# Kernel tuning notes

Measured on AMD Instinct MI355X. Metric: run time of the kernel, lower is better.

## Reference

```python
import jax, jax.numpy as jnp
import numpy as np

NUM_FEATURES = 35
BLANK = 2          # local blank index inside each 3-way category
NEG = -1e30        # finite stand-in for -inf (keeps grads NaN-free)


def _ctc_losses(log_probs, ext, skip_ok, valid, input_lengths, target_lengths):
    """Batched CTC negative log-likelihood.
    log_probs: [T,B,F,3] log-softmax per category
    ext:       [B,F,L] extended label sequence (blank interleaved), L=2S+1
    skip_ok:   [B,F,L] whether the l-2 transition is allowed
    valid:     [B,F,L] positions within 2*target_len+1
    Returns per-(B,F) loss.
    """
    T = log_probs.shape[0]

    emit0 = jnp.take_along_axis(log_probs[0], ext, axis=-1)  # [B,F,L]
    alpha = jnp.full_like(emit0, NEG)
    alpha = alpha.at[..., 0].set(emit0[..., 0])
    alpha = alpha.at[..., 1].set(jnp.where(target_lengths > 0, emit0[..., 1], NEG))

    pad1 = jnp.full(alpha.shape[:-1] + (1,), NEG, alpha.dtype)
    pad2 = jnp.full(alpha.shape[:-1] + (2,), NEG, alpha.dtype)

    def step(alpha, xs):
        lp_t, t = xs                                   # lp_t: [B,F,3]
        emit = jnp.take_along_axis(lp_t, ext, axis=-1)  # [B,F,L]
        a1 = jnp.concatenate([pad1, alpha[..., :-1]], axis=-1)
        a2 = jnp.concatenate([pad2, alpha[..., :-2]], axis=-1)
        prev = jnp.logaddexp(jnp.logaddexp(alpha, a1),
                             jnp.where(skip_ok, a2, NEG))
        new = jnp.where(valid, prev + emit, NEG)
        active = (t < input_lengths)[:, None, None]     # [B,1,1]
        return jnp.where(active, new, alpha), None

    alpha, _ = jax.lax.scan(step, alpha, (log_probs[1:], jnp.arange(1, T)))

    idx_last = 2 * target_lengths                       # [B,F] final blank
    last = jnp.take_along_axis(alpha, idx_last[..., None], axis=-1)[..., 0]
    prev_ = jnp.take_along_axis(alpha, jnp.maximum(idx_last - 1, 0)[..., None], axis=-1)[..., 0]
    prev_ = jnp.where(target_lengths > 0, prev_, NEG)
    ll = jnp.logaddexp(last, prev_)
    # zero_infinity=True: impossible alignments contribute 0 loss
    return jnp.where(ll > -1e29, -ll, 0.0)


def reference(logits, targets, input_lengths, target_lengths):
    # logits: [T,B,71]; targets: [B,35,S] local labels in {0,1};
    # input_lengths: [B]; target_lengths: [B,35]
    T, B, _ = logits.shape
    F = NUM_FEATURES
    pos = logits[:, :, :F]
    neg = logits[:, :, F:2 * F]
    blank = jnp.broadcast_to(logits[:, :, 2 * F:2 * F + 1], pos.shape)
    lp = jax.nn.log_softmax(jnp.stack([pos, neg, blank], axis=-1), axis=-1)  # [T,B,F,3]

    S = targets.shape[-1]
    L = 2 * S + 1
    ext = jnp.full((B, F, L), BLANK, jnp.int32).at[:, :, 1::2].set(targets.astype(jnp.int32))
    posL = jnp.arange(L)
    valid = posL[None, None, :] < (2 * target_lengths[..., None] + 1)
    ext_m2 = jnp.pad(ext[:, :, :-2], ((0, 0), (0, 0), (2, 0)), constant_values=BLANK)
    skip_ok = (ext != BLANK) & (ext != ext_m2) & (posL[None, None, :] >= 2)

    loss_bf = _ctc_losses(lp, ext, skip_ok, valid, input_lengths, target_lengths)  # [B,F]
    # reduction='mean': per-sample loss divided by its target length, averaged over batch,
    # then summed over the 35 feature categories (the python loop accumulates per-feature means)
    tl = jnp.maximum(target_lengths, 1).astype(loss_bf.dtype)
    return jnp.sum(jnp.mean(loss_bf / tl, axis=0))


def setup_inputs() -> dict:
    T, B, S = 600, 32, 80
    key = jax.random.key(0)
    k1, k2, k3 = jax.random.split(key, 3)
    logits = jax.random.normal(k1, (T, B, 2 * NUM_FEATURES + 1), dtype=jnp.float32)
    targets = jax.random.randint(k2, (B, NUM_FEATURES, S), 0, 2, dtype=jnp.int32)
    target_lengths = jax.random.randint(k3, (B, NUM_FEATURES), 40, S + 1, dtype=jnp.int32)
    input_lengths = jnp.full((B,), T, dtype=jnp.int32)
    return {"logits": logits, "targets": targets,
            "input_lengths": input_lengths, "target_lengths": target_lengths}
```

## Files before the change

### kernel.cpp

```cpp
#include <hip/hip_runtime.h>

#define LN2 0.6931471805599453f

typedef float f32x4 __attribute__((ext_vector_type(4)));

__device__ __forceinline__ float dpp_shr1_zero(float x) {
    return __int_as_float(__builtin_amdgcn_update_dpp(
        0, __float_as_int(x), 0x138, 0xF, 0xF, true));
}
__device__ __forceinline__ int dpp_shr1_keep(int x) {
    return __builtin_amdgcn_update_dpp(x, x, 0x138, 0xF, 0xF, false);
}
__device__ __forceinline__ float dpp_shl1_zero(float x) {
    return __int_as_float(__builtin_amdgcn_update_dpp(
        0, __float_as_int(x), 0x130, 0xF, 0xF, true));
}
__device__ __forceinline__ int dpp_shl1_keep(int x) {
    return __builtin_amdgcn_update_dpp(x, x, 0x130, 0xF, 0xF, false);
}
__device__ __forceinline__ float exp2i_clamped(int d) {
    int k = 127 + d;
    k = (k < 1) ? 1 : ((k > 254) ? 254 : k);
    return __uint_as_float(((unsigned)k) << 23);
}

struct FwdState {
    float a0, a1, a2;
    float s1, k0, k1;
    int   esum;
};
struct BwdState {
    float c0, c1, c2;
    float s1b, kA, kB;
    int   esum;
};

__device__ __forceinline__ void fwd_step(float em0, float em1, float em2,
                                         FwdState& st, float skm2) {
    float d2 = dpp_shr1_zero(st.a2);
    float d1 = dpp_shr1_zero(st.a1);
    float n0 = fmaf(st.k0, d1, fmaf(st.s1, d2, st.a0)) * em0;
    float n1 = fmaf(st.k1, d2, st.a1 + st.a0) * em1;
    float n2 = fmaf(skm2, st.a0, st.a2 + st.a1) * em2;
    st.a0 = n0; st.a1 = n1; st.a2 = n2;
}
__device__ __forceinline__ void bwd_step(float em0, float em1, float em2,
                                         BwdState& st, float skm2) {
    float d3 = dpp_shl1_zero(st.c0);
    float d4 = dpp_shl1_zero(st.c1);
    float n0 = fmaf(skm2, st.c2, st.c0 + st.c1) * em0;
    float n1 = fmaf(st.kA, d3, st.c1 + st.c2) * em1;
    float n2 = fmaf(st.kB, d4, fmaf(st.s1b, d3, st.c2)) * em2;
    st.c0 = n0; st.c1 = n1; st.c2 = n2;
}

__device__ __forceinline__ void fwd_rescale(FwdState& st, float skm0, float skm1) {
    float m = fmaxf(fmaxf(st.a0, st.a1), st.a2);
    int ebits = (int)(__float_as_uint(m) >> 23);
    bool dead = (ebits == 0);
    int de = dead ? 0 : (127 - ebits);
    float scz = dead ? 0.0f : exp2i_clamped(de);
    st.a0 *= scz; st.a1 *= scz; st.a2 *= scz;
    st.esum -= de;
    #pragma unroll
    for (int r = 0; r < 5; ++r) {
        int en = dpp_shr1_keep(st.esum);
        st.esum = dead ? en : st.esum;
    }
    int enf = dpp_shr1_keep(st.esum);
    int gap = enf - st.esum;
    int adj = (gap > 64) ? (gap - 64) : 0;
    float sc3 = exp2i_clamped(-adj);
    st.a0 *= sc3; st.a1 *= sc3; st.a2 *= sc3;
    st.esum += adj;
    st.s1 = exp2i_clamped(gap - adj);
    st.k0 = skm0 * st.s1;
    st.k1 = skm1 * st.s1;
}
__device__ __forceinline__ void bwd_rescale(BwdState& st, float sknA, float sknB) {
    float m = fmaxf(fmaxf(st.c0, st.c1), st.c2);
    int ebits = (int)(__float_as_uint(m) >> 23);
    bool dead = (ebits == 0);
    int de = dead ? 0 : (127 - ebits);
    float scz = dead ? 0.0f : exp2i_clamped(de);
    st.c0 *= scz; st.c1 *= scz; st.c2 *= scz;
    st.esum -= de;
    #pragma unroll
    for (int r = 0; r < 5; ++r) {
        int en = dpp_shl1_keep(st.esum);
        st.esum = dead ? en : st.esum;
    }
    #pragma unroll
    for (int r = 0; r < 3; ++r) {
        int enl = dpp_shr1_keep(st.esum);
        int mn = (enl < st.esum) ? enl : st.esum;
        st.esum = dead ? mn : st.esum;
    }
    int deadR = dpp_shl1_keep(dead ? 1 : 0);
    int enf = dpp_shl1_keep(st.esum);
    int gap = enf - st.esum;
    int adj = (gap > 64) ? (gap - 64) : 0;
    adj = (adj > 126) ? 126 : adj;
    adj = deadR ? 0 : adj;
    float sc3 = exp2i_clamped(-adj);
    st.c0 *= sc3; st.c1 *= sc3; st.c2 *= sc3;
    st.esum += adj;
    float s1b = exp2i_clamped(gap - adj);
    st.s1b = deadR ? 0.f : s1b;
    st.kA = sknA * st.s1b;
    st.kB = sknB * st.s1b;
}

__global__ __launch_bounds__(128, 1) void ctc_kernel(
    const float* __restrict__ logits,
    const int* __restrict__ targets,
    const int* __restrict__ input_lengths,
    const int* __restrict__ target_lengths,
    float* __restrict__ loss_out,
    int T, int B, int Ff, int S)
{
    const int p = blockIdx.x;
    const int b = p / Ff;
    const int f = p - b * Ff;
    const int tid = (int)threadIdx.x;
    const int wid = tid >> 6;
    const int lane = tid & 63;
    const int C = 2 * Ff + 1;
    const int L = 2 * S + 1;

    const int tl = target_lengths[p];
    const int il = input_lengths[b];
    const int tbase = p * S;

    float tf0, tf1, tf2, skm0, skm1, skm2;
    {
        float tf[3], sk[3];
        const int l0 = 3 * lane;
        #pragma unroll
        for (int j = 0; j < 3; ++j) {
            int l = l0 + j;
            float tv = 0.f, sok = 0.f;
            if (l < L && (l & 1)) {
                int s = (l - 1) >> 1;
                int ev = targets[tbase + s];
                tv = (float)ev;
                if (s >= 1) sok = (targets[tbase + s - 1] != ev) ? 1.f : 0.f;
            }
            tf[j] = tv; sk[j] = sok;
        }
        tf0 = tf[0]; tf1 = tf[1]; tf2 = tf[2];
        skm0 = sk[0]; skm1 = sk[1]; skm2 = sk[2];
    }
    const float sknA = dpp_shl1_zero(skm0);
    const float sknB = dpp_shl1_zero(skm1);
    const float vP = (float)(lane & 1);
    const float vQ = 1.0f - vP;

    __shared__ f32x4 slp[640];
    {
        const float* lg = logits + (size_t)b * C;
        const size_t strideT = (size_t)B * C;
        float c0 = 0.f, c1 = 0.f, c2 = 0.f;
        if (tid < T) {
            const float* r = lg + (size_t)tid * strideT;
            c0 = r[f]; c1 = r[Ff + f]; c2 = r[2 * Ff];
        }
        #pragma unroll 1
        for (int j = 0; j < 5; ++j) {
            int i = tid + (j << 7);
            int inx = i + 128;
            float n0 = 0.f, n1 = 0.f, n2 = 0.f;
            if (inx < T) {
                const float* r = lg + (size_t)inx * strideT;
                n0 = r[f]; n1 = r[Ff + f]; n2 = r[2 * Ff];
            }
            f32x4 v = {0.f, 0.f, 0.f, 0.f};
            if (i < T) {
                float m = fmaxf(fmaxf(c0, c1), c2);
                float ep = __expf(c0 - m);
                float en = __expf(c1 - m);
                float eb = __expf(c2 - m);
                float inv = __builtin_amdgcn_rcpf(ep + en + eb);
                float p0 = ep * inv, p1 = en * inv, pb = eb * inv;
                v[0] = p1 - p0; v[1] = p0 - pb; v[2] = pb;
            }
            if (i < 640) slp[i] = v;
            c0 = n0; c1 = n1; c2 = n2;
        }
    }
    __syncthreads();

    const int TL = (il < T) ? il : T;
    const int m_ = (TL >= 2) ? ((TL - 1) >> 1) : 0;
    const int Fn = m_;
    const int Bk = (TL >= 2) ? (TL - 2 - m_) : 0;

    __shared__ float sa[192];
    __shared__ float sg[194];
    __shared__ int   seb[65];
    __shared__ float sdot[64];
    __shared__ int   sE[64];

#define EMF(E, EV0, EV1, EV2) \
    float iA = fmaf(vP, (E)[1], (E)[2]); \
    float iB = fmaf(vQ, (E)[1], (E)[2]); \
    float EV0 = fmaf(tf0, (E)[0], iA); \
    float EV1 = fmaf(tf1, (E)[0], iB); \
    float EV2 = fmaf(tf2, (E)[0], iA);

    FwdState fs;
    fs.a0 = 0.f; fs.a1 = 0.f; fs.a2 = 0.f; fs.s1 = 1.f;
    fs.k0 = skm0; fs.k1 = skm1; fs.esum = 0;

    if (wid == 0) {
        {
            f32x4 E0 = slp[0];
            float e1i0 = fmaf(tf1, E0[0], E0[1] + E0[2]);
            fs.a0 = (lane == 0) ? E0[2] : 0.f;
            fs.a1 = (lane == 0 && tl > 0) ? e1i0 : 0.f;
            fs.a2 = 0.f;
        }
        const int t_endF = Fn + 1;
        int t = 1;
#define FSTEP(IDX) { f32x4 E = slp[(IDX)]; EMF(E, e0, e1, e2) \
                     fwd_step(e0, e1, e2, fs, skm2); }
        #pragma unroll 1
        for (; t + 16 <= t_endF; t += 16) {
            fwd_rescale(fs, skm0, skm1);
            FSTEP(t)      FSTEP(t + 1)  FSTEP(t + 2)  FSTEP(t + 3)
            FSTEP(t + 4)  FSTEP(t + 5)  FSTEP(t + 6)  FSTEP(t + 7)
            fwd_rescale(fs, skm0, skm1);
            FSTEP(t + 8)  FSTEP(t + 9)  FSTEP(t + 10) FSTEP(t + 11)
            FSTEP(t + 12) FSTEP(t + 13) FSTEP(t + 14) FSTEP(t + 15)
        }
        #pragma unroll 1
        for (; t < t_endF; ++t) FSTEP(t)
#undef FSTEP
        {
            int l = 3 * lane;
            sa[l] = fs.a0; sa[l + 1] = fs.a1; sa[l + 2] = fs.a2;
        }
    } else {
        BwdState bs;
        {
            f32x4 EL = slp[TL - 1];
            EMF(EL, eL0, eL1, eL2)
            int l0i = 3 * lane;
            int end1 = 2 * tl, end2 = 2 * tl - 1;
            bs.c0 = (l0i == end1 || l0i == end2) ? eL0 : 0.f;
            bs.c1 = (l0i + 1 == end1 || l0i + 1 == end2) ? eL1 : 0.f;
            bs.c2 = (l0i + 2 == end1 || l0i + 2 == end2) ? eL2 : 0.f;
            bs.s1b = 1.f; bs.kA = sknA; bs.kB = sknB;
            bs.esum = 0;
        }
        int k = 0;
        int tr = TL - 2;
#define BSTEP(IDX) { f32x4 E = slp[(IDX)]; EMF(E, e0, e1, e2) \
                     bwd_step(e0, e1, e2, bs, skm2); }
        #pragma unroll 1
        for (; k + 16 <= Bk; k += 16, tr -= 16) {
            bwd_rescale(bs, sknA, sknB);
            BSTEP(tr)      BSTEP(tr - 1)  BSTEP(tr - 2)  BSTEP(tr - 3)
            BSTEP(tr - 4)  BSTEP(tr - 5)  BSTEP(tr - 6)  BSTEP(tr - 7)
            bwd_rescale(bs, sknA, sknB);
            BSTEP(tr - 8)  BSTEP(tr - 9)  BSTEP(tr - 10) BSTEP(tr - 11)
            BSTEP(tr - 12) BSTEP(tr - 13) BSTEP(tr - 14) BSTEP(tr - 15)
        }
        #pragma unroll 1
        for (; k < Bk; ++k, --tr) BSTEP(tr)
#undef BSTEP
        {
            int l = 3 * lane;
            sg[l] = bs.c0; sg[l + 1] = bs.c1; sg[l + 2] = bs.c2;
            seb[lane] = bs.esum;
            if (lane == 0) { sg[192] = 0.f; sg[193] = 0.f; seb[64] = 0; }
        }
    }
    __syncthreads();

    if (wid == 0) {
        int eB = seb[lane];
        float scn = exp2i_clamped(seb[lane + 1] - eB);
        float g0 = sg[3 * lane], g1 = sg[3 * lane + 1], g2 = sg[3 * lane + 2];
        float g3 = sg[3 * lane + 3] * scn;
        float g4 = sg[3 * lane + 4] * scn;
        float s0 = fmaf(skm2, g2, g0 + g1);
        float s1v = fmaf(sknA, g3, g1 + g2);
        float s2v = fmaf(sknB, g4, g2 + g3);
        float dot = fs.a0 * s0 + fs.a1 * s1v + fs.a2 * s2v;
        sdot[lane] = dot;
        sE[lane] = fs.esum + eB;
    }
    __syncthreads();
    if (tid == 0) {
        float loss = 0.f;
        if (TL == 1) {
            float v = sa[2 * tl] + ((tl > 0) ? sa[2 * tl - 1] : 0.f);
            if (v > 0.f) loss = -(__log2f(v) * LN2);
        } else {
            int Emax = -0x40000000;
            for (int i = 0; i < 64; ++i)
                if (sdot[i] > 0.f && sE[i] > Emax) Emax = sE[i];
            if (Emax != -0x40000000) {
                float sum = 0.f;
                for (int i = 0; i < 64; ++i) {
                    int d = sE[i] - Emax;
                    if (d > -127 && sdot[i] > 0.f) sum += sdot[i] * exp2i_clamped(d);
                }
                loss = -((__log2f(sum) + (float)Emax) * LN2);
            }
        }
        float denom = (tl > 0) ? (float)tl : 1.0f;
        loss_out[p] = loss / denom;
    }
#undef EMF
}

__global__ __launch_bounds__(256) void reduce_kernel(
    const float* __restrict__ v, float* __restrict__ out, int n, float invB)
{
    __shared__ float buf[256];
    float s = 0.f;
    for (int i = (int)threadIdx.x; i < n; i += 256) s += v[i];
    buf[threadIdx.x] = s;
    __syncthreads();
    for (int off = 128; off > 0; off >>= 1) {
        if ((int)threadIdx.x < off) buf[threadIdx.x] += buf[threadIdx.x + off];
        __syncthreads();
    }
    if (threadIdx.x == 0) out[0] = buf[0] * invB;
}

extern "C" void kernel_launch(void* const* d_in, const int* in_sizes, int n_in,
                              void* d_out, int out_size, void* d_ws, size_t ws_size,
                              hipStream_t stream) {
    const float* logits         = (const float*)d_in[0];
    const int*   targets        = (const int*)d_in[1];
    const int*   input_lengths  = (const int*)d_in[2];
    const int*   target_lengths = (const int*)d_in[3];
    float* out = (float*)d_out;

    const int B  = in_sizes[2];
    const int BF = in_sizes[3];
    const int Ff = BF / B;
    const int S  = in_sizes[1] / BF;
    const int C  = 2 * Ff + 1;
    const int T  = in_sizes[0] / (B * C);

    float* losses = (float*)d_ws;

    ctc_kernel<<<BF, 128, 0, stream>>>(logits, targets, input_lengths,
                                       target_lengths, losses, T, B, Ff, S);
    reduce_kernel<<<1, 256, 0, stream>>>(losses, out, BF, 1.0f / (float)B);
}
```

Baseline: 60.42 us.

## Keep per-timestep probabilities in registers and broadcast via readlane instead of LDS

Removes the shared-memory staging of per-timestep softmax values. Each wave now loads and computes only the 6x64 timesteps it needs into registers, and the serial forward and backward recurrences fetch each timestep's values with readlane broadcasts instead of LDS reads. This drops a block-wide barrier and the LDS load latency from the critical serial loop. The cost is more registers, scalar readlane traffic and a rescale every 8 steps instead of every 8 with the old 16-step unroll. It assumes each wave's range fits in 384 timesteps.

```diff
diff --git a/kernel.cpp b/kernel.cpp
--- a/kernel.cpp
+++ b/kernel.cpp
@@ -1,8 +1,6 @@
 #include <hip/hip_runtime.h>
 
 #define LN2 0.6931471805599453f
-
-typedef float f32x4 __attribute__((ext_vector_type(4)));
 
 __device__ __forceinline__ float dpp_shr1_zero(float x) {
     return __int_as_float(__builtin_amdgcn_update_dpp(
@@ -22,6 +20,9 @@
     int k = 127 + d;
     k = (k < 1) ? 1 : ((k > 254) ? 254 : k);
     return __uint_as_float(((unsigned)k) << 23);
+}
+__device__ __forceinline__ float rls(float v, int ln) {
+    return __int_as_float(__builtin_amdgcn_readlane(__float_as_int(v), ln));
 }
 
 struct FwdState {
@@ -156,44 +157,34 @@
     const float vP = (float)(lane & 1);
     const float vQ = 1.0f - vP;
 
-    __shared__ f32x4 slp[640];
+    const int TL = (il < T) ? il : T;
+    const int m_ = (TL >= 2) ? ((TL - 1) >> 1) : 0;
+    const int Fn = m_;
+
+    const int W0 = (wid == 0) ? 0 : ((m_ + 1) >> 6);
+    float qd[6], qq[6], qb[6];
     {
         const float* lg = logits + (size_t)b * C;
         const size_t strideT = (size_t)B * C;
-        float c0 = 0.f, c1 = 0.f, c2 = 0.f;
-        if (tid < T) {
-            const float* r = lg + (size_t)tid * strideT;
-            c0 = r[f]; c1 = r[Ff + f]; c2 = r[2 * Ff];
-        }
-        #pragma unroll 1
-        for (int j = 0; j < 5; ++j) {
-            int i = tid + (j << 7);
-            int inx = i + 128;
-            float n0 = 0.f, n1 = 0.f, n2 = 0.f;
-            if (inx < T) {
-                const float* r = lg + (size_t)inx * strideT;
-                n0 = r[f]; n1 = r[Ff + f]; n2 = r[2 * Ff];
-            }
-            f32x4 v = {0.f, 0.f, 0.f, 0.f};
-            if (i < T) {
-                float m = fmaxf(fmaxf(c0, c1), c2);
-                float ep = __expf(c0 - m);
-                float en = __expf(c1 - m);
-                float eb = __expf(c2 - m);
-                float inv = __builtin_amdgcn_rcpf(ep + en + eb);
-                float p0 = ep * inv, p1 = en * inv, pb = eb * inv;
-                v[0] = p1 - p0; v[1] = p0 - pb; v[2] = pb;
-            }
-            if (i < 640) slp[i] = v;
-            c0 = n0; c1 = n1; c2 = n2;
-        }
-    }
-    __syncthreads();
-
-    const int TL = (il < T) ? il : T;
-    const int m_ = (TL >= 2) ? ((TL - 1) >> 1) : 0;
-    const int Fn = m_;
-    const int Bk = (TL >= 2) ? (TL - 2 - m_) : 0;
+        float r0[6], r1[6], r2[6];
+        #pragma unroll
+        for (int w = 0; w < 6; ++w) {
+            int row = ((W0 + w) << 6) + lane;
+            int rc = (row < T) ? row : 0;
+            const float* r = lg + (size_t)rc * strideT;
+            r0[w] = r[f]; r1[w] = r[Ff + f]; r2[w] = r[2 * Ff];
+        }
+        #pragma unroll
+        for (int w = 0; w < 6; ++w) {
+            float m = fmaxf(fmaxf(r0[w], r1[w]), r2[w]);
+            float ep = __expf(r0[w] - m);
+            float en = __expf(r1[w] - m);
+            float eb = __expf(r2[w] - m);
+            float inv = __builtin_amdgcn_rcpf(ep + en + eb);
+            float p0 = ep * inv, p1 = en * inv, pb = eb * inv;
+            qd[w] = p1 - p0; qq[w] = p0 - pb; qb[w] = pb;
+        }
+    }
 
     __shared__ float sa[192];
     __shared__ float sg[194];
@@ -201,40 +192,49 @@
     __shared__ float sdot[64];
     __shared__ int   sE[64];
 
-#define EMF(E, EV0, EV1, EV2) \
-    float iA = fmaf(vP, (E)[1], (E)[2]); \
-    float iB = fmaf(vQ, (E)[1], (E)[2]); \
-    float EV0 = fmaf(tf0, (E)[0], iA); \
-    float EV1 = fmaf(tf1, (E)[0], iB); \
-    float EV2 = fmaf(tf2, (E)[0], iA);
-
     FwdState fs;
     fs.a0 = 0.f; fs.a1 = 0.f; fs.a2 = 0.f; fs.s1 = 1.f;
     fs.k0 = skm0; fs.k1 = skm1; fs.esum = 0;
 
     if (wid == 0) {
         {
-            f32x4 E0 = slp[0];
-            float e1i0 = fmaf(tf1, E0[0], E0[1] + E0[2]);
-            fs.a0 = (lane == 0) ? E0[2] : 0.f;
+            float d0v = rls(qd[0], 0), q0v = rls(qq[0], 0), b0v = rls(qb[0], 0);
+            float e1i0 = fmaf(tf1, d0v, q0v + b0v);
+            fs.a0 = (lane == 0) ? b0v : 0.f;
             fs.a1 = (lane == 0 && tl > 0) ? e1i0 : 0.f;
             fs.a2 = 0.f;
         }
-        const int t_endF = Fn + 1;
-        int t = 1;
-#define FSTEP(IDX) { f32x4 E = slp[(IDX)]; EMF(E, e0, e1, e2) \
-                     fwd_step(e0, e1, e2, fs, skm2); }
-        #pragma unroll 1
-        for (; t + 16 <= t_endF; t += 16) {
-            fwd_rescale(fs, skm0, skm1);
-            FSTEP(t)      FSTEP(t + 1)  FSTEP(t + 2)  FSTEP(t + 3)
-            FSTEP(t + 4)  FSTEP(t + 5)  FSTEP(t + 6)  FSTEP(t + 7)
-            fwd_rescale(fs, skm0, skm1);
-            FSTEP(t + 8)  FSTEP(t + 9)  FSTEP(t + 10) FSTEP(t + 11)
-            FSTEP(t + 12) FSTEP(t + 13) FSTEP(t + 14) FSTEP(t + 15)
-        }
-        #pragma unroll 1
-        for (; t < t_endF; ++t) FSTEP(t)
+#define FSTEP(W) { \
+    float sdv = rls(qd[W], s); \
+    float sqv = rls(qq[W], s); \
+    float sbv = rls(qb[W], s); \
+    float iA = fmaf(vP, sqv, sbv); \
+    float iB = fmaf(vQ, sqv, sbv); \
+    fwd_step(fmaf(tf0, sdv, iA), fmaf(tf1, sdv, iB), fmaf(tf2, sdv, iA), \
+             fs, skm2); \
+    ++s; }
+        #pragma unroll
+        for (int w = 0; w < 6; ++w) {
+            int base = w << 6;
+            int lo = (base > 1) ? base : 1;
+            int hi = base + 63; if (hi > Fn) hi = Fn;
+            int n = hi - lo + 1;
+            if (n > 0) {
+                int s = lo - base;
+                int i = 0;
+                #pragma unroll 1
+                for (; i + 8 <= n; i += 8) {
+                    fwd_rescale(fs, skm0, skm1);
+                    FSTEP(w) FSTEP(w) FSTEP(w) FSTEP(w)
+                    FSTEP(w) FSTEP(w) FSTEP(w) FSTEP(w)
+                }
+                if (i < n) {
+                    fwd_rescale(fs, skm0, skm1);
+                    #pragma unroll 1
+                    for (; i < n; ++i) FSTEP(w)
+                }
+            }
+        }
 #undef FSTEP
         {
             int l = 3 * lane;
@@ -243,8 +243,18 @@
     } else {
         BwdState bs;
         {
-            f32x4 EL = slp[TL - 1];
-            EMF(EL, eL0, eL1, eL2)
+            int wi = ((TL - 1) >> 6) - W0;
+            int li = (TL - 1) & 63;
+            float dv = 0.f, qv = 0.f, bv = 0.f;
+            #pragma unroll
+            for (int w = 0; w < 6; ++w) {
+                if (w == wi) { dv = rls(qd[w], li); qv = rls(qq[w], li); bv = rls(qb[w], li); }
+            }
+            float iA = fmaf(vP, qv, bv);
+            float iB = fmaf(vQ, qv, bv);
+            float eL0 = fmaf(tf0, dv, iA);
+            float eL1 = fmaf(tf1, dv, iB);
+            float eL2 = fmaf(tf2, dv, iA);
             int l0i = 3 * lane;
             int end1 = 2 * tl, end2 = 2 * tl - 1;
             bs.c0 = (l0i == end1 || l0i == end2) ? eL0 : 0.f;
@@ -253,21 +263,37 @@
             bs.s1b = 1.f; bs.kA = sknA; bs.kB = sknB;
             bs.esum = 0;
         }
-        int k = 0;
-        int tr = TL - 2;
-#define BSTEP(IDX) { f32x4 E = slp[(IDX)]; EMF(E, e0, e1, e2) \
-                     bwd_step(e0, e1, e2, bs, skm2); }
-        #pragma unroll 1
-        for (; k + 16 <= Bk; k += 16, tr -= 16) {
-            bwd_rescale(bs, sknA, sknB);
-            BSTEP(tr)      BSTEP(tr - 1)  BSTEP(tr - 2)  BSTEP(tr - 3)
-            BSTEP(tr - 4)  BSTEP(tr - 5)  BSTEP(tr - 6)  BSTEP(tr - 7)
-            bwd_rescale(bs, sknA, sknB);
-            BSTEP(tr - 8)  BSTEP(tr - 9)  BSTEP(tr - 10) BSTEP(tr - 11)
-            BSTEP(tr - 12) BSTEP(tr - 13) BSTEP(tr - 14) BSTEP(tr - 15)
-        }
-        #pragma unroll 1
-        for (; k < Bk; ++k, --tr) BSTEP(tr)
+#define BSTEP(W) { \
+    float sdv = rls(qd[W], s); \
+    float sqv = rls(qq[W], s); \
+    float sbv = rls(qb[W], s); \
+    float iA = fmaf(vP, sqv, sbv); \
+    float iB = fmaf(vQ, sqv, sbv); \
+    bwd_step(fmaf(tf0, sdv, iA), fmaf(tf1, sdv, iB), fmaf(tf2, sdv, iA), \
+             bs, skm2); \
+    --s; }
+        #pragma unroll
+        for (int w = 5; w >= 0; --w) {
+            int base = (W0 + w) << 6;
+            int hi = base + 63; if (hi > TL - 2) hi = TL - 2;
+            int lo = base; if (lo < m_ + 1) lo = m_ + 1;
+            int n = hi - lo + 1;
+            if (n > 0) {
+                int s = hi - base;
+                int i = 0;
+                #pragma unroll 1
+                for (; i + 8 <= n; i += 8) {
+                    bwd_rescale(bs, sknA, sknB);
+                    BSTEP(w) BSTEP(w) BSTEP(w) BSTEP(w)
+                    BSTEP(w) BSTEP(w) BSTEP(w) BSTEP(w)
+                }
+                if (i < n) {
+                    bwd_rescale(bs, sknA, sknB);
+                    #pragma unroll 1
+                    for (; i < n; ++i) BSTEP(w)
+                }
+            }
+        }
 #undef BSTEP
         {
             int l = 3 * lane;
@@ -313,7 +339,6 @@
         float denom = (tl > 0) ? (float)tl : 1.0f;
         loss_out[p] = loss / denom;
     }
-#undef EMF
 }
 
 __global__ __launch_bounds__(256) void reduce_kernel(
```

Result: slower. 74.36 us (+23.1%).

## Split softmax into separate kernel and stream emissions from global memory

Applied to the files above, without the earlier changes.

Moves the per-category 3-way softmax out of the CTC kernel into a dedicated fully-parallel kernel that writes float4 emission records to workspace. The CTC kernel then drops its shared-memory staging and the barrier, and instead loads 8 timesteps of emissions per iteration directly from global memory into registers, rescaling every 8 steps. This removes the serialized prologue that loaded strided logits before the recurrence could start. In exchange it adds a kernel launch, about 2.7 MB of workspace traffic, and global-load latency inside the sequential loop.

```diff
diff --git a/kernel.cpp b/kernel.cpp
--- a/kernel.cpp
+++ b/kernel.cpp
@@ -1,8 +1,6 @@
 #include <hip/hip_runtime.h>
 
 #define LN2 0.6931471805599453f
-
-typedef float f32x4 __attribute__((ext_vector_type(4)));
 
 __device__ __forceinline__ float dpp_shr1_zero(float x) {
     return __int_as_float(__builtin_amdgcn_update_dpp(
@@ -111,8 +109,28 @@
     st.kB = sknB * st.s1b;
 }
 
+__global__ __launch_bounds__(256) void softmax_kernel(
+    const float* __restrict__ logits, float4* __restrict__ prec,
+    int T, int B, int Ff, int total)
+{
+    int g = blockIdx.x * 256 + (int)threadIdx.x;
+    if (g >= total) return;
+    int p = g / T, t = g - p * T;
+    int b = p / Ff, f = p - b * Ff;
+    int C = 2 * Ff + 1;
+    const float* r = logits + ((size_t)t * B + b) * C;
+    float xp = r[f], xn = r[Ff + f], xb = r[2 * Ff];
+    float m = fmaxf(fmaxf(xp, xn), xb);
+    float ep = __expf(xp - m);
+    float en = __expf(xn - m);
+    float eb = __expf(xb - m);
+    float inv = __builtin_amdgcn_rcpf(ep + en + eb);
+    float p0 = ep * inv, p1 = en * inv, pb = eb * inv;
+    prec[g] = make_float4(p1 - p0, p0 - pb, pb, 0.f);
+}
+
 __global__ __launch_bounds__(128, 1) void ctc_kernel(
-    const float* __restrict__ logits,
+    const float4* __restrict__ prec,
     const int* __restrict__ targets,
     const int* __restrict__ input_lengths,
     const int* __restrict__ target_lengths,
@@ -121,11 +139,9 @@
 {
     const int p = blockIdx.x;
     const int b = p / Ff;
-    const int f = p - b * Ff;
     const int tid = (int)threadIdx.x;
-    const int wid = tid >> 6;
+    const int wid = __builtin_amdgcn_readfirstlane(tid >> 6);
     const int lane = tid & 63;
-    const int C = 2 * Ff + 1;
     const int L = 2 * S + 1;
 
     const int tl = target_lengths[p];
@@ -156,44 +172,12 @@
     const float vP = (float)(lane & 1);
     const float vQ = 1.0f - vP;
 
-    __shared__ f32x4 slp[640];
-    {
-        const float* lg = logits + (size_t)b * C;
-        const size_t strideT = (size_t)B * C;
-        float c0 = 0.f, c1 = 0.f, c2 = 0.f;
-        if (tid < T) {
-            const float* r = lg + (size_t)tid * strideT;
-            c0 = r[f]; c1 = r[Ff + f]; c2 = r[2 * Ff];
-        }
-        #pragma unroll 1
-        for (int j = 0; j < 5; ++j) {
-            int i = tid + (j << 7);
-            int inx = i + 128;
-            float n0 = 0.f, n1 = 0.f, n2 = 0.f;
-            if (inx < T) {
-                const float* r = lg + (size_t)inx * strideT;
-                n0 = r[f]; n1 = r[Ff + f]; n2 = r[2 * Ff];
-            }
-            f32x4 v = {0.f, 0.f, 0.f, 0.f};
-            if (i < T) {
-                float m = fmaxf(fmaxf(c0, c1), c2);
-                float ep = __expf(c0 - m);
-                float en = __expf(c1 - m);
-                float eb = __expf(c2 - m);
-                float inv = __builtin_amdgcn_rcpf(ep + en + eb);
-                float p0 = ep * inv, p1 = en * inv, pb = eb * inv;
-                v[0] = p1 - p0; v[1] = p0 - pb; v[2] = pb;
-            }
-            if (i < 640) slp[i] = v;
-            c0 = n0; c1 = n1; c2 = n2;
-        }
-    }
-    __syncthreads();
-
     const int TL = (il < T) ? il : T;
     const int m_ = (TL >= 2) ? ((TL - 1) >> 1) : 0;
     const int Fn = m_;
     const int Bk = (TL >= 2) ? (TL - 2 - m_) : 0;
+
+    const float* pr = (const float*)(prec + (size_t)p * T);
 
     __shared__ float sa[192];
     __shared__ float sg[194];
@@ -201,41 +185,51 @@
     __shared__ float sdot[64];
     __shared__ int   sE[64];
 
-#define EMF(E, EV0, EV1, EV2) \
-    float iA = fmaf(vP, (E)[1], (E)[2]); \
-    float iB = fmaf(vQ, (E)[1], (E)[2]); \
-    float EV0 = fmaf(tf0, (E)[0], iA); \
-    float EV1 = fmaf(tf1, (E)[0], iB); \
-    float EV2 = fmaf(tf2, (E)[0], iA);
-
     FwdState fs;
     fs.a0 = 0.f; fs.a1 = 0.f; fs.a2 = 0.f; fs.s1 = 1.f;
     fs.k0 = skm0; fs.k1 = skm1; fs.esum = 0;
 
+#define EMIT_STEP_F(SD, SQ, SB) { \
+    float vpb = (SB); \
+    float iA = fmaf(vP, (SQ), vpb); \
+    float iB = fmaf(vQ, (SQ), vpb); \
+    fwd_step(fmaf(tf0, (SD), iA), fmaf(tf1, (SD), iB), fmaf(tf2, (SD), iA), \
+             fs, skm2); }
+#define EMIT_STEP_B(SD, SQ, SB) { \
+    float vpb = (SB); \
+    float iA = fmaf(vP, (SQ), vpb); \
+    float iB = fmaf(vQ, (SQ), vpb); \
+    bwd_step(fmaf(tf0, (SD), iA), fmaf(tf1, (SD), iB), fmaf(tf2, (SD), iA), \
+             bs, skm2); }
+
     if (wid == 0) {
         {
-            f32x4 E0 = slp[0];
-            float e1i0 = fmaf(tf1, E0[0], E0[1] + E0[2]);
-            fs.a0 = (lane == 0) ? E0[2] : 0.f;
+            float d0v = pr[0], q0v = pr[1], b0v = pr[2];
+            float e1i0 = fmaf(tf1, d0v, q0v + b0v);
+            fs.a0 = (lane == 0) ? b0v : 0.f;
             fs.a1 = (lane == 0 && tl > 0) ? e1i0 : 0.f;
             fs.a2 = 0.f;
         }
         const int t_endF = Fn + 1;
         int t = 1;
-#define FSTEP(IDX) { f32x4 E = slp[(IDX)]; EMF(E, e0, e1, e2) \
-                     fwd_step(e0, e1, e2, fs, skm2); }
         #pragma unroll 1
-        for (; t + 16 <= t_endF; t += 16) {
+        for (; t + 8 <= t_endF; t += 8) {
+            float e[32];
+            #pragma unroll
+            for (int j = 0; j < 32; ++j) e[j] = pr[4 * t + j];
             fwd_rescale(fs, skm0, skm1);
-            FSTEP(t)      FSTEP(t + 1)  FSTEP(t + 2)  FSTEP(t + 3)
-            FSTEP(t + 4)  FSTEP(t + 5)  FSTEP(t + 6)  FSTEP(t + 7)
+            #pragma unroll
+            for (int k = 0; k < 8; ++k)
+                EMIT_STEP_F(e[4 * k], e[4 * k + 1], e[4 * k + 2])
+        }
+        if (t < t_endF) {
             fwd_rescale(fs, skm0, skm1);
-            FSTEP(t + 8)  FSTEP(t + 9)  FSTEP(t + 10) FSTEP(t + 11)
-            FSTEP(t + 12) FSTEP(t + 13) FSTEP(t + 14) FSTEP(t + 15)
-        }
-        #pragma unroll 1
-        for (; t < t_endF; ++t) FSTEP(t)
-#undef FSTEP
+            #pragma unroll 1
+            for (; t < t_endF; ++t) {
+                float sdv = pr[4 * t], sqv = pr[4 * t + 1], sbv = pr[4 * t + 2];
+                EMIT_STEP_F(sdv, sqv, sbv)
+            }
+        }
         {
             int l = 3 * lane;
             sa[l] = fs.a0; sa[l + 1] = fs.a1; sa[l + 2] = fs.a2;
@@ -243,8 +237,14 @@
     } else {
         BwdState bs;
         {
-            f32x4 EL = slp[TL - 1];
-            EMF(EL, eL0, eL1, eL2)
+            int rL = TL - 1;
+            float dv = pr[4 * rL], qv = pr[4 * rL + 1], bv = pr[4 * rL + 2];
+            float vpb = bv;
+            float iA = fmaf(vP, qv, vpb);
+            float iB = fmaf(vQ, qv, vpb);
+            float eL0 = fmaf(tf0, dv, iA);
+            float eL1 = fmaf(tf1, dv, iB);
+            float eL2 = fmaf(tf2, dv, iA);
             int l0i = 3 * lane;
             int end1 = 2 * tl, end2 = 2 * tl - 1;
             bs.c0 = (l0i == end1 || l0i == end2) ? eL0 : 0.f;
@@ -255,20 +255,25 @@
         }
         int k = 0;
         int tr = TL - 2;
-#define BSTEP(IDX) { f32x4 E = slp[(IDX)]; EMF(E, e0, e1, e2) \
-                     bwd_step(e0, e1, e2, bs, skm2); }
         #pragma unroll 1
-        for (; k + 16 <= Bk; k += 16, tr -= 16) {
+        for (; k + 8 <= Bk; k += 8, tr -= 8) {
+            float e[32];
+            int basev = 4 * (tr - 7);
+            #pragma unroll
+            for (int j = 0; j < 32; ++j) e[j] = pr[basev + j];
             bwd_rescale(bs, sknA, sknB);
-            BSTEP(tr)      BSTEP(tr - 1)  BSTEP(tr - 2)  BSTEP(tr - 3)
-            BSTEP(tr - 4)  BSTEP(tr - 5)  BSTEP(tr - 6)  BSTEP(tr - 7)
+            #pragma unroll
+            for (int q = 7; q >= 0; --q)
+                EMIT_STEP_B(e[4 * q], e[4 * q + 1], e[4 * q + 2])
+        }
+        if (k < Bk) {
             bwd_rescale(bs, sknA, sknB);
-            BSTEP(tr - 8)  BSTEP(tr - 9)  BSTEP(tr - 10) BSTEP(tr - 11)
-            BSTEP(tr - 12) BSTEP(tr - 13) BSTEP(tr - 14) BSTEP(tr - 15)
-        }
-        #pragma unroll 1
-        for (; k < Bk; ++k, --tr) BSTEP(tr)
-#undef BSTEP
+            #pragma unroll 1
+            for (; k < Bk; ++k, --tr) {
+                float sdv = pr[4 * tr], sqv = pr[4 * tr + 1], sbv = pr[4 * tr + 2];
+                EMIT_STEP_B(sdv, sqv, sbv)
+            }
+        }
         {
             int l = 3 * lane;
             sg[l] = bs.c0; sg[l + 1] = bs.c1; sg[l + 2] = bs.c2;
@@ -276,6 +281,8 @@
             if (lane == 0) { sg[192] = 0.f; sg[193] = 0.f; seb[64] = 0; }
         }
     }
+#undef EMIT_STEP_F
+#undef EMIT_STEP_B
     __syncthreads();
 
     if (wid == 0) {
@@ -313,7 +320,6 @@
         float denom = (tl > 0) ? (float)tl : 1.0f;
         loss_out[p] = loss / denom;
     }
-#undef EMF
 }
 
 __global__ __launch_bounds__(256) void reduce_kernel(
@@ -347,9 +353,13 @@
     const int C  = 2 * Ff + 1;
     const int T  = in_sizes[0] / (B * C);
 
-    float* losses = (float*)d_ws;
-
-    ctc_kernel<<<BF, 128, 0, stream>>>(logits, targets, input_lengths,
+    float*  losses = (float*)d_ws;
+    float4* prec   = (float4*)((char*)d_ws + 16384);
+
+    int total = BF * T;
+    softmax_kernel<<<(total + 255) / 256, 256, 0, stream>>>(
+        logits, prec, T, B, Ff, total);
+    ctc_kernel<<<BF, 128, 0, stream>>>(prec, targets, input_lengths,
                                        target_lengths, losses, T, B, Ff, S);
     reduce_kernel<<<1, 256, 0, stream>>>(losses, out, BF, 1.0f / (float)B);
 }
```

Result: slower. 85.79 us (+42.0%).
